# Kernel tuning notes

Measured on AMD Instinct MI355X. Metric: run time of the kernel, lower is better.

Reference implementation:

```python
import jax, jax.numpy as jnp
import numpy as np

H = 50  # hidden_size

def setup_inputs() -> dict:
    key = jax.random.key(0)
    ks = jax.random.split(key, 7)
    B, T, I = 8192, 2048, 1
    s_ih = 1.0 / np.sqrt(H)
    x = jax.random.normal(ks[0], (B, T, I), dtype=jnp.float32)
    # PyTorch nn.LSTM params, gate order (i, f, g, o)
    W_ih = jax.random.uniform(ks[1], (4 * H, I), minval=-s_ih, maxval=s_ih, dtype=jnp.float32)
    W_hh = jax.random.uniform(ks[2], (4 * H, H), minval=-s_ih, maxval=s_ih, dtype=jnp.float32)
    b_ih = jax.random.uniform(ks[3], (4 * H,), minval=-s_ih, maxval=s_ih, dtype=jnp.float32)
    b_hh = jax.random.uniform(ks[4], (4 * H,), minval=-s_ih, maxval=s_ih, dtype=jnp.float32)
    W_lin = jax.random.uniform(ks[5], (1, H), minval=-s_ih, maxval=s_ih, dtype=jnp.float32)
    b_lin = jax.random.uniform(ks[6], (1,), minval=-s_ih, maxval=s_ih, dtype=jnp.float32)
    return {"x": x, "W_ih": W_ih, "W_hh": W_hh, "b_ih": b_ih, "b_hh": b_hh,
            "W_lin": W_lin, "b_lin": b_lin}

def _lstm_last_h(x, W_ih, W_hh, b_ih, b_hh):
    B = x.shape[0]
    # precompute input contribution per timestep: [T, B, 4H]
    xg = jnp.einsum('bti,gi->tbg', x, W_ih) + (b_ih + b_hh)  # [T,B,4H]

    def step(carry, xg_t):
        h, c = carry
        z = xg_t + h @ W_hh.T  # [B,4H]
        i = jax.nn.sigmoid(z[:, :H])
        f = jax.nn.sigmoid(z[:, H:2 * H])
        g = jnp.tanh(z[:, 2 * H:3 * H])
        o = jax.nn.sigmoid(z[:, 3 * H:])
        c = f * c + i * g
        h = o * jnp.tanh(c)
        return (h, c), None

    h0 = jnp.zeros((B, H), dtype=x.dtype)
    c0 = jnp.zeros((B, H), dtype=x.dtype)
    (h_last, _), _ = jax.lax.scan(step, (h0, c0), xg)
    return h_last  # [B,H]

def reference(x, W_ih, W_hh, b_ih, b_hh, W_lin, b_lin):
    h_last = _lstm_last_h(x, W_ih, W_hh, b_ih, b_hh)
    return h_last @ W_lin.T + b_lin  # [B,1]
```

## Files before the change

kernel.cpp:

```cpp
#include <hip/hip_runtime.h>


#define HID   50
#define NSTEP 2048
#define GPB   2
#define BPB   32
#define HSTR  72

typedef _Float16 half8   __attribute__((ext_vector_type(8)));
typedef float    float4v __attribute__((ext_vector_type(4)));

__device__ __forceinline__ float gate_pair(float zi, float zf, float zg, float zo,
                                           float& c) {
    float ei = __builtin_amdgcn_exp2f(zi);
    float ef = __builtin_amdgcn_exp2f(zf);
    float Eg = __builtin_amdgcn_exp2f(zg);
    float eo = __builtin_amdgcn_exp2f(zo);
    float t1  = (1.0f + ei) * (1.0f + Eg);
    float num = c * t1 + (1.0f + ef) * (Eg - 1.0f);
    float D   = t1 * (1.0f + ef);
    c = num * __builtin_amdgcn_rcpf(D);
    float a  = fminf(fmaxf(2.8853900817779268f * c, -24.0f), 24.0f);
    float Ec = __builtin_amdgcn_exp2f(a);
    return (Ec - 1.0f) * __builtin_amdgcn_rcpf((1.0f + eo) * (1.0f + Ec));
}

__global__ __launch_bounds__(512, 2) void lstm_fused(
    const float* __restrict__ x,
    const float* __restrict__ W_ih,
    const float* __restrict__ W_hh,
    const float* __restrict__ b_ih,
    const float* __restrict__ b_hh,
    const float* __restrict__ W_lin,
    const float* __restrict__ b_lin,
    float* __restrict__ out)
{
    __shared__ __align__(16) _Float16 hbuf[GPB][2][16][HSTR];

    const int tid  = threadIdx.x;
    const int wave = tid >> 6;
    const int lane = tid & 63;
    const int col  = lane & 15;
    const int quad = lane >> 4;
    const int grp  = wave >> 2;
    const int jt   = wave & 3;
    const int b0   = blockIdx.x * BPB;
    const int j    = jt * 16 + col;

    for (int i = tid; i < GPB * 2 * 16 * HSTR; i += 512)
        (&hbuf[0][0][0][0])[i] = (_Float16)0.0f;
    __syncthreads();
    if (tid < BPB) {
        int g = tid >> 4, r = tid & 15;
        hbuf[g][0][r][HID]     = (_Float16)x[(size_t)(b0 + tid) * NSTEP];
        hbuf[g][0][r][HID + 1] = (_Float16)1.0f;
        hbuf[g][1][r][HID + 1] = (_Float16)1.0f;
    }

    const float LOG2E = 1.4426950408889634f;
    half8 bfrag[4][2];
    for (int g = 0; g < 4; ++g) {
        const float sc = (g == 2) ? (2.0f * LOG2E) : (-LOG2E);
        for (int kt = 0; kt < 2; ++kt) {
            half8 f;
            #pragma unroll
            for (int jj = 0; jj < 8; ++jj) {
                int k = kt * 32 + quad * 8 + jj;
                float v = 0.0f;
                if (j < HID) {
                    int row = g * HID + j;
                    if (k < HID)           v = W_hh[row * HID + k];
                    else if (k == HID)     v = W_ih[row];
                    else if (k == HID + 1) v = b_ih[row] + b_hh[row];
                }
                f[jj] = (_Float16)(v * sc);
            }
            bfrag[g][kt] = f;
        }
    }

    float c[4] = {0.f, 0.f, 0.f, 0.f};
    const bool xloader = (jt == 3) && (quad == 0);
    const float* xrow = x + (size_t)(b0 + grp * 16 + col) * NSTEP;
    const float4v Z4 = {0.f, 0.f, 0.f, 0.f};

    __syncthreads();

    for (int t = 0; t < NSTEP; ++t) {
        const int cur = t & 1;
        const int nxt = cur ^ 1;

        float xn = 0.f;
        if (xloader) {
            int tt = (t + 1 < NSTEP) ? (t + 1) : (NSTEP - 1);
            xn = xrow[tt];
        }

        const _Float16* arow = &hbuf[grp][cur][col][0];
        half8 a0 = *(const half8*)(arow + quad * 8);
        half8 a1 = *(const half8*)(arow + 32 + quad * 8);

        float4v d0, d1, d2, d3;
        d0 = __builtin_amdgcn_mfma_f32_16x16x32_f16(a0, bfrag[0][0], Z4, 0, 0, 0);
        d1 = __builtin_amdgcn_mfma_f32_16x16x32_f16(a0, bfrag[1][0], Z4, 0, 0, 0);
        d2 = __builtin_amdgcn_mfma_f32_16x16x32_f16(a0, bfrag[2][0], Z4, 0, 0, 0);
        d3 = __builtin_amdgcn_mfma_f32_16x16x32_f16(a0, bfrag[3][0], Z4, 0, 0, 0);
        d0 = __builtin_amdgcn_mfma_f32_16x16x32_f16(a1, bfrag[0][1], d0, 0, 0, 0);
        d1 = __builtin_amdgcn_mfma_f32_16x16x32_f16(a1, bfrag[1][1], d1, 0, 0, 0);
        d2 = __builtin_amdgcn_mfma_f32_16x16x32_f16(a1, bfrag[2][1], d2, 0, 0, 0);
        d3 = __builtin_amdgcn_mfma_f32_16x16x32_f16(a1, bfrag[3][1], d3, 0, 0, 0);

        _Float16 hv[4];
        #pragma unroll
        for (int r = 0; r < 4; ++r)
            hv[r] = (_Float16)gate_pair(d0[r], d1[r], d2[r], d3[r], c[r]);

        if (j < HID) {
            #pragma unroll
            for (int r = 0; r < 4; ++r)
                hbuf[grp][nxt][quad * 4 + r][j] = hv[r];
        }
        if (xloader)
            hbuf[grp][nxt][col][HID] = (_Float16)xn;

        __syncthreads();
    }

    if (tid < BPB) {
        int g = tid >> 4, r = tid & 15;
        float s = b_lin[0];
        for (int k = 0; k < HID; ++k)
            s += (float)hbuf[g][0][r][k] * W_lin[k];
        out[b0 + tid] = s;
    }
}

extern "C" void kernel_launch(void* const* d_in, const int* in_sizes, int n_in,
                              void* d_out, int out_size, void* d_ws, size_t ws_size,
                              hipStream_t stream) {
    const float* x     = (const float*)d_in[0];
    const float* W_ih  = (const float*)d_in[1];
    const float* W_hh  = (const float*)d_in[2];
    const float* b_ih  = (const float*)d_in[3];
    const float* b_hh  = (const float*)d_in[4];
    const float* W_lin = (const float*)d_in[5];
    const float* b_lin = (const float*)d_in[6];
    float* outp = (float*)d_out;
    dim3 grid(8192 / BPB), block(512);
    hipLaunchKernelGGL(lstm_fused, grid, block, 0, stream,
                       x, W_ih, W_hh, b_ih, b_hh, W_lin, b_lin, outp);
}
```

Baseline: 1.434 ms.

## Give each wave its own 4 batch rows and drop block barriers

Restructures the LSTM so each wave owns 4 batch rows and computes all 4 hidden-column tiles itself, keeping its hidden state in a private LDS slice. This removes the per-timestep __syncthreads and the LDS double buffer. The cost is 4x more MFMAs per wave, most of them spent on padding rows since only 4 of 16 A rows are real, plus 64 B-fragment registers per lane. The grid grows to 512 blocks of 256 threads. Correctness within a step relies on wave-lockstep LDS ordering: all lanes read A before anyone writes h, and the compiler must keep that order.

New measurement: 1.935 ms. +35.0%, slower.

```diff
diff --git a/kernel.cpp b/kernel.cpp
--- a/kernel.cpp
+++ b/kernel.cpp
@@ -3,8 +3,7 @@
 
 #define HID   50
 #define NSTEP 2048
-#define GPB   2
-#define BPB   32
+#define RPW   4
 #define HSTR  72
 
 typedef _Float16 half8   __attribute__((ext_vector_type(8)));
@@ -25,7 +24,7 @@
     return (Ec - 1.0f) * __builtin_amdgcn_rcpf((1.0f + eo) * (1.0f + Ec));
 }
 
-__global__ __launch_bounds__(512, 2) void lstm_fused(
+__global__ __launch_bounds__(256, 2) void lstm_fused(
     const float* __restrict__ x,
     const float* __restrict__ W_ih,
     const float* __restrict__ W_hh,
@@ -35,103 +34,92 @@
     const float* __restrict__ b_lin,
     float* __restrict__ out)
 {
-    __shared__ __align__(16) _Float16 hbuf[GPB][2][16][HSTR];
+    __shared__ __align__(16) _Float16 hbuf[4][16][HSTR];
 
     const int tid  = threadIdx.x;
     const int wave = tid >> 6;
     const int lane = tid & 63;
     const int col  = lane & 15;
     const int quad = lane >> 4;
-    const int grp  = wave >> 2;
-    const int jt   = wave & 3;
-    const int b0   = blockIdx.x * BPB;
-    const int j    = jt * 16 + col;
+    const int b0   = blockIdx.x * 16 + wave * RPW;
+    _Float16 (*hb)[HSTR] = hbuf[wave];
+    const int hrow = 4 * quad;
 
-    for (int i = tid; i < GPB * 2 * 16 * HSTR; i += 512)
-        (&hbuf[0][0][0][0])[i] = (_Float16)0.0f;
-    __syncthreads();
-    if (tid < BPB) {
-        int g = tid >> 4, r = tid & 15;
-        hbuf[g][0][r][HID]     = (_Float16)x[(size_t)(b0 + tid) * NSTEP];
-        hbuf[g][0][r][HID + 1] = (_Float16)1.0f;
-        hbuf[g][1][r][HID + 1] = (_Float16)1.0f;
+    for (int i = lane; i < 16 * HSTR; i += 64)
+        (&hb[0][0])[i] = (_Float16)0.0f;
+    if (col == 0) {
+        hb[hrow][HID]     = (_Float16)x[(size_t)(b0 + quad) * NSTEP];
+        hb[hrow][HID + 1] = (_Float16)1.0f;
     }
 
     const float LOG2E = 1.4426950408889634f;
-    half8 bfrag[4][2];
+    half8 bfrag[4][4][2];
     for (int g = 0; g < 4; ++g) {
         const float sc = (g == 2) ? (2.0f * LOG2E) : (-LOG2E);
-        for (int kt = 0; kt < 2; ++kt) {
-            half8 f;
-            #pragma unroll
-            for (int jj = 0; jj < 8; ++jj) {
-                int k = kt * 32 + quad * 8 + jj;
-                float v = 0.0f;
-                if (j < HID) {
-                    int row = g * HID + j;
-                    if (k < HID)           v = W_hh[row * HID + k];
-                    else if (k == HID)     v = W_ih[row];
-                    else if (k == HID + 1) v = b_ih[row] + b_hh[row];
+        for (int jt = 0; jt < 4; ++jt) {
+            const int j = jt * 16 + col;
+            for (int kt = 0; kt < 2; ++kt) {
+                half8 f;
+                #pragma unroll
+                for (int jj = 0; jj < 8; ++jj) {
+                    int k = kt * 32 + quad * 8 + jj;
+                    float v = 0.0f;
+                    if (j < HID) {
+                        int row = g * HID + j;
+                        if (k < HID)           v = W_hh[row * HID + k];
+                        else if (k == HID)     v = W_ih[row];
+                        else if (k == HID + 1) v = b_ih[row] + b_hh[row];
+                    }
+                    f[jj] = (_Float16)(v * sc);
                 }
-                f[jj] = (_Float16)(v * sc);
+                bfrag[g][jt][kt] = f;
             }
-            bfrag[g][kt] = f;
         }
     }
 
     float c[4] = {0.f, 0.f, 0.f, 0.f};
-    const bool xloader = (jt == 3) && (quad == 0);
-    const float* xrow = x + (size_t)(b0 + grp * 16 + col) * NSTEP;
+    const float* xrow = x + (size_t)(b0 + quad) * NSTEP;
     const float4v Z4 = {0.f, 0.f, 0.f, 0.f};
 
-    __syncthreads();
+#define MFMA16(A, B, C) __builtin_amdgcn_mfma_f32_16x16x32_f16(A, B, C, 0, 0, 0)
 
     for (int t = 0; t < NSTEP; ++t) {
-        const int cur = t & 1;
-        const int nxt = cur ^ 1;
-
         float xn = 0.f;
-        if (xloader) {
+        if (col == 0) {
             int tt = (t + 1 < NSTEP) ? (t + 1) : (NSTEP - 1);
             xn = xrow[tt];
         }
 
-        const _Float16* arow = &hbuf[grp][cur][col][0];
+        const _Float16* arow = &hb[col][0];
         half8 a0 = *(const half8*)(arow + quad * 8);
         half8 a1 = *(const half8*)(arow + 32 + quad * 8);
 
-        float4v d0, d1, d2, d3;
-        d0 = __builtin_amdgcn_mfma_f32_16x16x32_f16(a0, bfrag[0][0], Z4, 0, 0, 0);
-        d1 = __builtin_amdgcn_mfma_f32_16x16x32_f16(a0, bfrag[1][0], Z4, 0, 0, 0);
-        d2 = __builtin_amdgcn_mfma_f32_16x16x32_f16(a0, bfrag[2][0], Z4, 0, 0, 0);
-        d3 = __builtin_amdgcn_mfma_f32_16x16x32_f16(a0, bfrag[3][0], Z4, 0, 0, 0);
-        d0 = __builtin_amdgcn_mfma_f32_16x16x32_f16(a1, bfrag[0][1], d0, 0, 0, 0);
-        d1 = __builtin_amdgcn_mfma_f32_16x16x32_f16(a1, bfrag[1][1], d1, 0, 0, 0);
-        d2 = __builtin_amdgcn_mfma_f32_16x16x32_f16(a1, bfrag[2][1], d2, 0, 0, 0);
-        d3 = __builtin_amdgcn_mfma_f32_16x16x32_f16(a1, bfrag[3][1], d3, 0, 0, 0);
+        #pragma unroll
+        for (int jt = 0; jt < 4; ++jt) {
+            float4v d0, d1, d2, d3;
+            d0 = MFMA16(a0, bfrag[0][jt][0], Z4);
+            d1 = MFMA16(a0, bfrag[1][jt][0], Z4);
+            d2 = MFMA16(a0, bfrag[2][jt][0], Z4);
+            d3 = MFMA16(a0, bfrag[3][jt][0], Z4);
+            d0 = MFMA16(a1, bfrag[0][jt][1], d0);
+            d1 = MFMA16(a1, bfrag[1][jt][1], d1);
+            d2 = MFMA16(a1, bfrag[2][jt][1], d2);
+            d3 = MFMA16(a1, bfrag[3][jt][1], d3);
+            float h = gate_pair(d0[0], d1[0], d2[0], d3[0], c[jt]);
+            const int j = jt * 16 + col;
+            if (j < HID)
+                hb[hrow][j] = (_Float16)h;
+        }
+        if (col == 0)
+            hb[hrow][HID] = (_Float16)xn;
+    }
+#undef MFMA16
 
-        _Float16 hv[4];
-        #pragma unroll
-        for (int r = 0; r < 4; ++r)
-            hv[r] = (_Float16)gate_pair(d0[r], d1[r], d2[r], d3[r], c[r]);
-
-        if (j < HID) {
-            #pragma unroll
-            for (int r = 0; r < 4; ++r)
-                hbuf[grp][nxt][quad * 4 + r][j] = hv[r];
-        }
-        if (xloader)
-            hbuf[grp][nxt][col][HID] = (_Float16)xn;
-
-        __syncthreads();
-    }
-
-    if (tid < BPB) {
-        int g = tid >> 4, r = tid & 15;
+    if (col == 0) {
         float s = b_lin[0];
         for (int k = 0; k < HID; ++k)
-            s += (float)hbuf[g][0][r][k] * W_lin[k];
-        out[b0 + tid] = s;
+            s += (float)hb[hrow][k] * W_lin[k];
+        out[b0 + quad] = s;
     }
 }
 
@@ -146,7 +134,7 @@
     const float* W_lin = (const float*)d_in[5];
     const float* b_lin = (const float*)d_in[6];
     float* outp = (float*)d_out;
-    dim3 grid(8192 / BPB), block(512);
+    dim3 grid(8192 / 16), block(256);
     hipLaunchKernelGGL(lstm_fused, grid, block, 0, stream,
                        x, W_ih, W_hh, b_ih, b_hh, W_lin, b_lin, outp);
 }
```
